# Kernel optimization log

Hardware: AMD Instinct MI355X
Metric: run time of the kernel (lower is better)

## Reference

```python
import jax, jax.numpy as jnp
import numpy as np
import math

L, C, H, W = 5, 256, 128, 384

def _subset_masks(L):
    # For each agent i, enumerate all non-empty subsets S of the other L-1 agents.
    # masks[i, s, :] is the indicator of S union {i}; wgt[i, s] = |S|!(L-|S|-1)!/L!.
    S = 2 ** (L - 1) - 1
    masks = np.zeros((L, S, L), dtype=np.float32)
    wgt = np.zeros((L, S), dtype=np.float32)
    for i in range(L):
        others = [j for j in range(L) if j != i]
        for m in range(1, 2 ** (L - 1)):
            bits = [others[k] for k in range(L - 1) if (m >> k) & 1]
            card = len(bits)
            masks[i, m - 1, bits] = 1.0
            masks[i, m - 1, i] = 1.0
            wgt[i, m - 1] = math.factorial(card) * math.factorial(L - card - 1) / math.factorial(L)
    return masks, wgt

_MASKS, _WGT = _subset_masks(L)

def setup_inputs() -> dict:
    key = jax.random.key(0)
    k1, k2, k3 = jax.random.split(key, 3)
    feats = jax.random.normal(k1, (L, C, H, W), dtype=jnp.float32)
    bound = 1.0 / np.sqrt(C)  # nn.Linear default init scale
    w = jax.random.uniform(k2, (C, 1), dtype=jnp.float32, minval=-bound, maxval=bound)
    b = jax.random.uniform(k3, (1,), dtype=jnp.float32, minval=-bound, maxval=bound)
    return {"feats": feats, "w": w, "b": b}

def reference(feats, w, b):
    Lc, Cc, Hc, Wc = feats.shape
    N = Hc * Wc
    x = feats.reshape(Lc, Cc, N).transpose(0, 2, 1)  # (L, N, C) == rearrange 'l c h w -> l (h w) c'
    # Linear is affine, so lin(sum_j f_j) = sum_j (f_j @ w) + b. Precompute per-agent projections.
    z = jnp.einsum('lnc,co->ln', x, w)  # (L, N), no bias yet
    masks = jnp.asarray(_MASKS)  # (L, S, L)
    wgt = jnp.asarray(_WGT)      # (L, S)
    # ReLU(lin(sum over subset S u {i})) for every agent / subset, vectorized
    subset_val = jax.nn.relu(jnp.einsum('lsm,mn->lsn', masks, z) + b[0])  # (L, S, N)
    self_val = jax.nn.relu(z + b[0])  # (L, N) = contrib_feats_i
    # shapley[i] = sum_S w(|S|) * (v(S u {i}) - v({i})) + v({i}) / L
    shap = (jnp.einsum('ls,lsn->ln', wgt, subset_val)
            - jnp.sum(wgt, axis=1)[:, None] * self_val
            + self_val / Lc)  # (L, N)
    wsoft = jax.nn.softmax(shap, axis=0)  # softmax over agents
    out = jnp.einsum('lnc,ln->nc', x, wsoft)  # (N, C)
    return out.T.reshape(Cc, Hc, Wc)
```

## Files before the change

### kernel.cpp

```cpp
#include <hip/hip_runtime.h>

#define L 5
#define C 256
#define HH 128
#define WW 384
#define N (HH * WW)
#define TN 8
#define NBLK (N / TN)
#define ROWS (L * C)

__global__ __launch_bounds__(256) void k_fused(const float* __restrict__ feats,
                                               const float* __restrict__ w,
                                               const float* __restrict__ bptr,
                                               float* __restrict__ out) {
    __shared__ float tile[ROWS * TN];
    __shared__ float wlds[C];
    __shared__ float zl[L][TN];
    __shared__ float wsl[L][TN];

    const int t = threadIdx.x;

    const int blk = (blockIdx.x & 7) * (NBLK / 8) + (blockIdx.x >> 3);
    const int n0 = blk * TN;

    wlds[t] = w[t];
    if (t < L * TN) ((float*)zl)[t] = 0.f;
    __syncthreads();

    const float bv = bptr[0];
    const int n4 = t & 1;
    const int r0 = t >> 1;

    float za = 0.f, zb = 0.f, zc = 0.f, zd = 0.f;
#pragma unroll
    for (int k = 0; k < 10; ++k) {
        const int r = r0 + 128 * k;
        const int c = r & 255;
        const float4 v = *(const float4*)(feats + (size_t)r * N + n0 + n4 * 4);
        *(float4*)(&tile[(size_t)(t + 256 * k) * 4]) = v;
        const float wc = wlds[c];
        za += wc * v.x; zb += wc * v.y; zc += wc * v.z; zd += wc * v.w;
        if (k & 1) {
            float s0 = za, s1 = zb, s2 = zc, s3 = zd;
#pragma unroll
            for (int st = 2; st <= 32; st <<= 1) {
                s0 += __shfl_xor(s0, st);
                s1 += __shfl_xor(s1, st);
                s2 += __shfl_xor(s2, st);
                s3 += __shfl_xor(s3, st);
            }
            if ((t & 63) < 2) {
                const int l = k >> 1;
                const int nn = n4 * 4;
                atomicAdd(&zl[l][nn + 0], s0);
                atomicAdd(&zl[l][nn + 1], s1);
                atomicAdd(&zl[l][nn + 2], s2);
                atomicAdd(&zl[l][nn + 3], s3);
            }
            za = zb = zc = zd = 0.f;
        }
    }
    __syncthreads();

    if (t < TN) {
        float zv[L];
#pragma unroll
        for (int l = 0; l < L; ++l) zv[l] = zl[l][t];

        const float wcard[5] = {0.f, 0.05f, 1.f / 30.f, 0.05f, 0.2f};
        float shap[L];
#pragma unroll
        for (int i = 0; i < L; ++i) {
            int others[4];
            int kk = 0;
#pragma unroll
            for (int j = 0; j < L; ++j)
                if (j != i) others[kk++] = j;
            float acc = 0.f;
#pragma unroll
            for (int m = 1; m < 16; ++m) {
                float s = zv[i] + bv;
                int card = 0;
#pragma unroll
                for (int q = 0; q < 4; ++q)
                    if ((m >> q) & 1) { s += zv[others[q]]; ++card; }
                acc += wcard[card] * fmaxf(s, 0.f);
            }
            const float self = fmaxf(zv[i] + bv, 0.f);
            shap[i] = acc - 0.6f * self;
        }
        float mx = shap[0];
#pragma unroll
        for (int i = 1; i < L; ++i) mx = fmaxf(mx, shap[i]);
        float e[L], sum = 0.f;
#pragma unroll
        for (int i = 0; i < L; ++i) { e[i] = __expf(shap[i] - mx); sum += e[i]; }
        const float inv = 1.f / sum;
#pragma unroll
        for (int i = 0; i < L; ++i) wsl[i][t] = e[i] * inv;
    }
    __syncthreads();

    float wr[L][4];
#pragma unroll
    for (int l = 0; l < L; ++l)
#pragma unroll
        for (int j = 0; j < 4; ++j) wr[l][j] = wsl[l][n4 * 4 + j];

#pragma unroll
    for (int k2 = 0; k2 < 2; ++k2) {
        const int c = r0 + 128 * k2;
        float4 acc = make_float4(0.f, 0.f, 0.f, 0.f);
#pragma unroll
        for (int l = 0; l < L; ++l) {
            const float4 f = *(const float4*)(&tile[(size_t)(l * 512 + t + 256 * k2) * 4]);
            acc.x += f.x * wr[l][0];
            acc.y += f.y * wr[l][1];
            acc.z += f.z * wr[l][2];
            acc.w += f.w * wr[l][3];
        }
        *(float4*)(out + (size_t)c * N + n0 + n4 * 4) = acc;
    }
}

extern "C" void kernel_launch(void* const* d_in, const int* in_sizes, int n_in,
                              void* d_out, int out_size, void* d_ws, size_t ws_size,
                              hipStream_t stream) {
    const float* feats = (const float*)d_in[0];
    const float* w     = (const float*)d_in[1];
    const float* bptr  = (const float*)d_in[2];
    float* out = (float*)d_out;

    k_fused<<<NBLK, 256, 0, stream>>>(feats, w, bptr, out);
}
```

Baseline: 371.2 us.

## Stage feature tile in LDS as bf16 and double the pixel tile width

New measurement: 364.4 us. Within noise of the previous version (-1.8%).

```diff
diff --git a/kernel.cpp b/kernel.cpp
--- a/kernel.cpp
+++ b/kernel.cpp
@@ -5,15 +5,24 @@
 #define HH 128
 #define WW 384
 #define N (HH * WW)
-#define TN 8
+#define TN 16
 #define NBLK (N / TN)
 #define ROWS (L * C)
+
+__device__ __forceinline__ unsigned short bf16rne(float x) {
+    unsigned int u = __float_as_uint(x);
+    return (unsigned short)((u + 0x7FFFu + ((u >> 16) & 1u)) >> 16);
+}
+__device__ __forceinline__ float bf16tof(unsigned short h) {
+    unsigned int u = ((unsigned int)h) << 16;
+    return __uint_as_float(u);
+}
 
 __global__ __launch_bounds__(256) void k_fused(const float* __restrict__ feats,
                                                const float* __restrict__ w,
                                                const float* __restrict__ bptr,
                                                float* __restrict__ out) {
-    __shared__ float tile[ROWS * TN];
+    __shared__ unsigned short tile[ROWS * TN];
     __shared__ float wlds[C];
     __shared__ float zl[L][TN];
     __shared__ float wsl[L][TN];
@@ -28,30 +37,33 @@
     __syncthreads();
 
     const float bv = bptr[0];
-    const int n4 = t & 1;
-    const int r0 = t >> 1;
+    const int q = t & 3;
+    const int r0 = t >> 2;
 
     float za = 0.f, zb = 0.f, zc = 0.f, zd = 0.f;
 #pragma unroll
-    for (int k = 0; k < 10; ++k) {
-        const int r = r0 + 128 * k;
+    for (int k = 0; k < 20; ++k) {
+        const int r = r0 + 64 * k;
         const int c = r & 255;
-        const float4 v = *(const float4*)(feats + (size_t)r * N + n0 + n4 * 4);
-        *(float4*)(&tile[(size_t)(t + 256 * k) * 4]) = v;
+        const float4 v = *(const float4*)(feats + (size_t)r * N + n0 + q * 4);
+        ushort4 h;
+        h.x = bf16rne(v.x); h.y = bf16rne(v.y);
+        h.z = bf16rne(v.z); h.w = bf16rne(v.w);
+        *(ushort4*)(&tile[r * TN + q * 4]) = h;
         const float wc = wlds[c];
         za += wc * v.x; zb += wc * v.y; zc += wc * v.z; zd += wc * v.w;
-        if (k & 1) {
+        if ((k & 3) == 3) {
+            const int l = k >> 2;
             float s0 = za, s1 = zb, s2 = zc, s3 = zd;
 #pragma unroll
-            for (int st = 2; st <= 32; st <<= 1) {
+            for (int st = 4; st <= 32; st <<= 1) {
                 s0 += __shfl_xor(s0, st);
                 s1 += __shfl_xor(s1, st);
                 s2 += __shfl_xor(s2, st);
                 s3 += __shfl_xor(s3, st);
             }
-            if ((t & 63) < 2) {
-                const int l = k >> 1;
-                const int nn = n4 * 4;
+            if ((t & 63) < 4) {
+                const int nn = (t & 3) * 4;
                 atomicAdd(&zl[l][nn + 0], s0);
                 atomicAdd(&zl[l][nn + 1], s1);
                 atomicAdd(&zl[l][nn + 2], s2);
@@ -82,8 +94,8 @@
                 float s = zv[i] + bv;
                 int card = 0;
 #pragma unroll
-                for (int q = 0; q < 4; ++q)
-                    if ((m >> q) & 1) { s += zv[others[q]]; ++card; }
+                for (int p = 0; p < 4; ++p)
+                    if ((m >> p) & 1) { s += zv[others[p]]; ++card; }
                 acc += wcard[card] * fmaxf(s, 0.f);
             }
             const float self = fmaxf(zv[i] + bv, 0.f);
@@ -105,21 +117,21 @@
 #pragma unroll
     for (int l = 0; l < L; ++l)
 #pragma unroll
-        for (int j = 0; j < 4; ++j) wr[l][j] = wsl[l][n4 * 4 + j];
+        for (int j = 0; j < 4; ++j) wr[l][j] = wsl[l][q * 4 + j];
 
 #pragma unroll
-    for (int k2 = 0; k2 < 2; ++k2) {
-        const int c = r0 + 128 * k2;
+    for (int k2 = 0; k2 < 4; ++k2) {
+        const int c = r0 + 64 * k2;
         float4 acc = make_float4(0.f, 0.f, 0.f, 0.f);
 #pragma unroll
         for (int l = 0; l < L; ++l) {
-            const float4 f = *(const float4*)(&tile[(size_t)(l * 512 + t + 256 * k2) * 4]);
-            acc.x += f.x * wr[l][0];
-            acc.y += f.y * wr[l][1];
-            acc.z += f.z * wr[l][2];
-            acc.w += f.w * wr[l][3];
+            const ushort4 h = *(const ushort4*)(&tile[(l * 256 + c) * TN + q * 4]);
+            acc.x += bf16tof(h.x) * wr[l][0];
+            acc.y += bf16tof(h.y) * wr[l][1];
+            acc.z += bf16tof(h.z) * wr[l][2];
+            acc.w += bf16tof(h.w) * wr[l][3];
         }
-        *(float4*)(out + (size_t)c * N + n0 + n4 * 4) = acc;
+        *(float4*)(out + (size_t)c * N + n0 + q * 4) = acc;
     }
 }
 
```
